# Kernel tuning notes

Hardware: AMD Instinct MI355X
Metric: run time of the kernel (lower is better)

## Reference

```python
import jax, jax.numpy as jnp
import numpy as np

B, D_IN, D_H = 4096, 1024, 2048


def setup_inputs() -> dict:
    key = jax.random.key(0)
    ks = jax.random.split(key, 16)
    s_in = 1.0 / np.sqrt(D_IN)
    s_h = 1.0 / np.sqrt(D_H)
    inp = {
        "x": jax.random.normal(ks[0], (B, D_IN), jnp.float32),
        "h_prev": jax.random.normal(ks[1], (B, D_H), jnp.float32),
        "c_prev": jax.random.normal(ks[2], (B, D_H), jnp.float32),
        "n_prev": jax.random.uniform(ks[3], (B, D_H), jnp.float32) + 0.5,
        # input-gate weights [D_H, D_IN] (torch Linear layout) + biases
        "Wz": jax.random.uniform(ks[4], (D_H, D_IN), jnp.float32, -s_in, s_in),
        "Wi": jax.random.uniform(ks[5], (D_H, D_IN), jnp.float32, -s_in, s_in),
        "Wf": jax.random.uniform(ks[6], (D_H, D_IN), jnp.float32, -s_in, s_in),
        "Wo": jax.random.uniform(ks[7], (D_H, D_IN), jnp.float32, -s_in, s_in),
        "bz": jax.random.uniform(ks[8], (D_H,), jnp.float32, -s_in, s_in),
        "bi": jax.random.uniform(ks[9], (D_H,), jnp.float32, -s_in, s_in),
        "bf": jax.random.uniform(ks[10], (D_H,), jnp.float32, -s_in, s_in),
        "bo": jax.random.uniform(ks[11], (D_H,), jnp.float32, -s_in, s_in),
        # recurrent weights [D_H, D_H], bias-free
        "Rz": jax.random.uniform(ks[12], (D_H, D_H), jnp.float32, -s_h, s_h),
        "Ri": jax.random.uniform(ks[13], (D_H, D_H), jnp.float32, -s_h, s_h),
        "Rf": jax.random.uniform(ks[14], (D_H, D_H), jnp.float32, -s_h, s_h),
        "Ro": jax.random.uniform(ks[15], (D_H, D_H), jnp.float32, -s_h, s_h),
    }
    return inp


def reference(x, h_prev, c_prev, n_prev,
              Wz, Wi, Wf, Wo, bz, bi, bf, bo,
              Rz, Ri, Rf, Ro):
    # Fuse the 4 input GEMMs and 4 recurrent GEMMs into two batched contractions.
    Wcat = jnp.concatenate([Wz, Wi, Wf, Wo], axis=0)      # [4H, D_IN]
    Rcat = jnp.concatenate([Rz, Ri, Rf, Ro], axis=0)      # [4H, H]
    bcat = jnp.concatenate([bz, bi, bf, bo], axis=0)      # [4H]
    pre = x @ Wcat.T + h_prev @ Rcat.T + bcat              # [B, 4H]
    az, ai, af, ao = jnp.split(pre, 4, axis=1)
    z = jnp.tanh(az)
    i = jnp.exp(ai)
    f = jnp.exp(af)
    o = jax.nn.sigmoid(ao)
    c = f * c_prev + i * z
    n = f * n_prev + i
    h = o * (c / n)
    return h
```

## Files before the change

### kernel.cpp

```cpp
#include <hip/hip_runtime.h>
#include <hip/hip_fp16.h>

#define B_SZ  4096
#define DIN   1024
#define DH    2048
#define K_TOT 3072
#define N_TOT 8192

#define BM 128
#define BN 128
#define BK 32

typedef _Float16 half8 __attribute__((ext_vector_type(8)));
typedef float   float4v __attribute__((ext_vector_type(4)));

__device__ __forceinline__ void load_lds16(const void* g, void* l) {
    __builtin_amdgcn_global_load_lds(
        (const __attribute__((address_space(1))) void*)g,
        (__attribute__((address_space(3))) void*)l,
        16, 0, 0);
}

__global__ __launch_bounds__(256) void cast_A_kernel(
        const float* __restrict__ x, const float* __restrict__ h,
        _Float16* __restrict__ A) {
    int idx = (blockIdx.x * 256 + threadIdx.x) * 8;
    int b = idx / K_TOT;
    int c = idx - b * K_TOT;
    const float* src = (c < DIN) ? (x + (size_t)b * DIN + c)
                                 : (h + (size_t)b * DH + (c - DIN));
    float4 v0 = *reinterpret_cast<const float4*>(src);
    float4 v1 = *reinterpret_cast<const float4*>(src + 4);
    half8 o;
    o[0] = (_Float16)v0.x; o[1] = (_Float16)v0.y;
    o[2] = (_Float16)v0.z; o[3] = (_Float16)v0.w;
    o[4] = (_Float16)v1.x; o[5] = (_Float16)v1.y;
    o[6] = (_Float16)v1.z; o[7] = (_Float16)v1.w;
    *reinterpret_cast<half8*>(A + idx) = o;
}

__global__ __launch_bounds__(256) void cast_W_kernel(
        const float* __restrict__ Wz, const float* __restrict__ Wi,
        const float* __restrict__ Wf, const float* __restrict__ Wo,
        const float* __restrict__ Rz, const float* __restrict__ Ri,
        const float* __restrict__ Rf, const float* __restrict__ Ro,
        _Float16* __restrict__ Wb) {
    int idx = (blockIdx.x * 256 + threadIdx.x) * 8;
    int n = idx / K_TOT;
    int c = idx - n * K_TOT;
    int t = n & 127;
    int g = (t >> 4) & 3;
    int j = ((n >> 7) << 5) + ((t >> 6) << 4) + (t & 15);
    const float* W = (g == 0) ? Wz : (g == 1) ? Wi : (g == 2) ? Wf : Wo;
    const float* R = (g == 0) ? Rz : (g == 1) ? Ri : (g == 2) ? Rf : Ro;
    const float* src = (c < DIN) ? (W + (size_t)j * DIN + c)
                                 : (R + (size_t)j * DH + (c - DIN));
    float4 v0 = *reinterpret_cast<const float4*>(src);
    float4 v1 = *reinterpret_cast<const float4*>(src + 4);
    half8 o;
    o[0] = (_Float16)v0.x; o[1] = (_Float16)v0.y;
    o[2] = (_Float16)v0.z; o[3] = (_Float16)v0.w;
    o[4] = (_Float16)v1.x; o[5] = (_Float16)v1.y;
    o[6] = (_Float16)v1.z; o[7] = (_Float16)v1.w;
    *reinterpret_cast<half8*>(Wb + idx) = o;
}

__global__ __launch_bounds__(256) void slstm_gemm_kernel(
        const _Float16* __restrict__ A, const _Float16* __restrict__ Wb,
        const float* __restrict__ c_prev, const float* __restrict__ n_prev,
        const float* __restrict__ bz, const float* __restrict__ bi,
        const float* __restrict__ bf, const float* __restrict__ bo,
        float* __restrict__ Hout) {
    __shared__ __align__(16) _Float16 As[BM * BK];
    __shared__ __align__(16) _Float16 Bs[BN * BK];

    const int ntile = blockIdx.x;
    const int mtile = blockIdx.y;
    const int tid  = threadIdx.x;
    const int wv   = tid >> 6;
    const int wm   = wv >> 1;
    const int wn   = wv & 1;
    const int l    = tid & 63;
    const int quad = l >> 4;
    const int l16  = l & 15;

    const int m0 = mtile * BM;
    const int n0 = ntile * BN;

    float4v acc[4][4];
#pragma unroll
    for (int i = 0; i < 4; i++)
#pragma unroll
        for (int j = 0; j < 4; j++) acc[i][j] = (float4v){0.f, 0.f, 0.f, 0.f};

    const int chunk0 = wv * 2;
    const int srow0  = chunk0 * 16 + (l >> 2);
    const int srow1  = srow0 + 16;
    const int skoff  = (((l & 3) ^ ((l >> 3) & 3)) * 8);

    const _Float16* Ag0 = A  + (size_t)(m0 + srow0) * K_TOT + skoff;
    const _Float16* Ag1 = A  + (size_t)(m0 + srow1) * K_TOT + skoff;
    const _Float16* Bg0 = Wb + (size_t)(n0 + srow0) * K_TOT + skoff;
    const _Float16* Bg1 = Wb + (size_t)(n0 + srow1) * K_TOT + skoff;

    _Float16* AsL0 = As + chunk0 * 512;
    _Float16* AsL1 = As + (chunk0 + 1) * 512;
    _Float16* BsL0 = Bs + chunk0 * 512;
    _Float16* BsL1 = Bs + (chunk0 + 1) * 512;

    const int kq = (quad ^ ((l16 >> 1) & 3)) * 8;

    for (int kt = 0; kt < K_TOT; kt += BK) {
        load_lds16(Ag0 + kt, AsL0);
        load_lds16(Ag1 + kt, AsL1);
        load_lds16(Bg0 + kt, BsL0);
        load_lds16(Bg1 + kt, BsL1);
        __syncthreads();

        half8 afr[4], bfr[4];
#pragma unroll
        for (int mf = 0; mf < 4; mf++)
            afr[mf] = *reinterpret_cast<const half8*>(As + (wm * 64 + mf * 16 + l16) * BK + kq);
#pragma unroll
        for (int nf = 0; nf < 4; nf++)
            bfr[nf] = *reinterpret_cast<const half8*>(Bs + (wn * 64 + nf * 16 + l16) * BK + kq);

#pragma unroll
        for (int mf = 0; mf < 4; mf++)
#pragma unroll
            for (int nf = 0; nf < 4; nf++)
                acc[mf][nf] = __builtin_amdgcn_mfma_f32_16x16x32_f16(afr[mf], bfr[nf], acc[mf][nf], 0, 0, 0);
        __syncthreads();
    }

    const int j = ntile * 32 + wn * 16 + l16;
    const float bzv = bz[j], biv = bi[j], bfv = bf[j], bov = bo[j];
#pragma unroll
    for (int mf = 0; mf < 4; mf++) {
#pragma unroll
        for (int r = 0; r < 4; r++) {
            const int row = m0 + wm * 64 + mf * 16 + quad * 4 + r;
            const size_t off = (size_t)row * DH + j;
            const float az  = acc[mf][0][r] + bzv;
            const float ai  = acc[mf][1][r] + biv;
            const float af_ = acc[mf][2][r] + bfv;
            const float ao  = acc[mf][3][r] + bov;
            const float ax = fabsf(az);
            const float e2 = __expf(-2.0f * ax);
            float tz = __fdividef(1.0f - e2, 1.0f + e2);
            tz = (az >= 0.0f) ? tz : -tz;
            const float iv = __expf(ai);
            const float fv = __expf(af_);
            const float ov = __fdividef(1.0f, 1.0f + __expf(-ao));
            const float cc = fv * c_prev[off] + iv * tz;
            const float nn = fv * n_prev[off] + iv;
            Hout[off] = ov * __fdividef(cc, nn);
        }
    }
}

extern "C" void kernel_launch(void* const* d_in, const int* in_sizes, int n_in,
                              void* d_out, int out_size, void* d_ws, size_t ws_size,
                              hipStream_t stream) {
    const float* x      = (const float*)d_in[0];
    const float* h_prev = (const float*)d_in[1];
    const float* c_prev = (const float*)d_in[2];
    const float* n_prev = (const float*)d_in[3];
    const float* Wz = (const float*)d_in[4];
    const float* Wi = (const float*)d_in[5];
    const float* Wf = (const float*)d_in[6];
    const float* Wo = (const float*)d_in[7];
    const float* bz = (const float*)d_in[8];
    const float* bi = (const float*)d_in[9];
    const float* bf = (const float*)d_in[10];
    const float* bo = (const float*)d_in[11];
    const float* Rz = (const float*)d_in[12];
    const float* Ri = (const float*)d_in[13];
    const float* Rf = (const float*)d_in[14];
    const float* Ro = (const float*)d_in[15];

    _Float16* A  = (_Float16*)d_ws;
    _Float16* Wb = A + (size_t)B_SZ * K_TOT;

    cast_A_kernel<<<(B_SZ * K_TOT / 8) / 256, 256, 0, stream>>>(x, h_prev, A);
    cast_W_kernel<<<(N_TOT * K_TOT / 8) / 256, 256, 0, stream>>>(
        Wz, Wi, Wf, Wo, Rz, Ri, Rf, Ro, Wb);

    dim3 grid(N_TOT / BN, B_SZ / BM);
    slstm_gemm_kernel<<<grid, 256, 0, stream>>>(
        A, Wb, c_prev, n_prev, bz, bi, bf, bo, (float*)d_out);
}
```

Measured before the change: 478.6 us.

## Double GEMM K-tile to 64 with 8-way swizzle and merge cast kernels

The GEMM K-step grows from 32 to 64. Each wave now issues four direct-to-LDS loads per operand, and a new 8-way XOR swizzle matches the wider rows. This halves the number of barrier pairs per K sweep and gives each sync twice as many MFMAs, at the cost of doubling LDS use (32KB per block). The two fp32-to-fp16 cast kernels are also merged into one launch, removing a kernel boundary.

```diff
diff --git a/kernel.cpp b/kernel.cpp
--- a/kernel.cpp
+++ b/kernel.cpp
@@ -9,7 +9,7 @@
 
 #define BM 128
 #define BN 128
-#define BK 32
+#define BK 64
 
 typedef _Float16 half8 __attribute__((ext_vector_type(8)));
 typedef float   float4v __attribute__((ext_vector_type(4)));
@@ -21,14 +21,36 @@
         16, 0, 0);
 }
 
-__global__ __launch_bounds__(256) void cast_A_kernel(
+#define A_BLOCKS ((B_SZ * K_TOT / 8) / 256)
+#define W_BLOCKS ((N_TOT * K_TOT / 8) / 256)
+
+__global__ __launch_bounds__(256) void cast_all_kernel(
         const float* __restrict__ x, const float* __restrict__ h,
-        _Float16* __restrict__ A) {
-    int idx = (blockIdx.x * 256 + threadIdx.x) * 8;
-    int b = idx / K_TOT;
-    int c = idx - b * K_TOT;
-    const float* src = (c < DIN) ? (x + (size_t)b * DIN + c)
-                                 : (h + (size_t)b * DH + (c - DIN));
+        const float* __restrict__ Wz, const float* __restrict__ Wi,
+        const float* __restrict__ Wf, const float* __restrict__ Wo,
+        const float* __restrict__ Rz, const float* __restrict__ Ri,
+        const float* __restrict__ Rf, const float* __restrict__ Ro,
+        _Float16* __restrict__ A, _Float16* __restrict__ Wb) {
+    const float* src;
+    _Float16* dst;
+    if (blockIdx.x < A_BLOCKS) {
+        int idx = (blockIdx.x * 256 + threadIdx.x) * 8;
+        int b = idx / K_TOT;
+        int c = idx - b * K_TOT;
+        src = (c < DIN) ? (x + (size_t)b * DIN + c) : (h + (size_t)b * DH + (c - DIN));
+        dst = A + idx;
+    } else {
+        int idx = ((blockIdx.x - A_BLOCKS) * 256 + threadIdx.x) * 8;
+        int n = idx / K_TOT;
+        int c = idx - n * K_TOT;
+        int t = n & 127;
+        int g = (t >> 4) & 3;
+        int j = ((n >> 7) << 5) + ((t >> 6) << 4) + (t & 15);
+        const float* W = (g == 0) ? Wz : (g == 1) ? Wi : (g == 2) ? Wf : Wo;
+        const float* R = (g == 0) ? Rz : (g == 1) ? Ri : (g == 2) ? Rf : Ro;
+        src = (c < DIN) ? (W + (size_t)j * DIN + c) : (R + (size_t)j * DH + (c - DIN));
+        dst = Wb + idx;
+    }
     float4 v0 = *reinterpret_cast<const float4*>(src);
     float4 v1 = *reinterpret_cast<const float4*>(src + 4);
     half8 o;
@@ -36,33 +58,7 @@
     o[2] = (_Float16)v0.z; o[3] = (_Float16)v0.w;
     o[4] = (_Float16)v1.x; o[5] = (_Float16)v1.y;
     o[6] = (_Float16)v1.z; o[7] = (_Float16)v1.w;
-    *reinterpret_cast<half8*>(A + idx) = o;
-}
-
-__global__ __launch_bounds__(256) void cast_W_kernel(
-        const float* __restrict__ Wz, const float* __restrict__ Wi,
-        const float* __restrict__ Wf, const float* __restrict__ Wo,
-        const float* __restrict__ Rz, const float* __restrict__ Ri,
-        const float* __restrict__ Rf, const float* __restrict__ Ro,
-        _Float16* __restrict__ Wb) {
-    int idx = (blockIdx.x * 256 + threadIdx.x) * 8;
-    int n = idx / K_TOT;
-    int c = idx - n * K_TOT;
-    int t = n & 127;
-    int g = (t >> 4) & 3;
-    int j = ((n >> 7) << 5) + ((t >> 6) << 4) + (t & 15);
-    const float* W = (g == 0) ? Wz : (g == 1) ? Wi : (g == 2) ? Wf : Wo;
-    const float* R = (g == 0) ? Rz : (g == 1) ? Ri : (g == 2) ? Rf : Ro;
-    const float* src = (c < DIN) ? (W + (size_t)j * DIN + c)
-                                 : (R + (size_t)j * DH + (c - DIN));
-    float4 v0 = *reinterpret_cast<const float4*>(src);
-    float4 v1 = *reinterpret_cast<const float4*>(src + 4);
-    half8 o;
-    o[0] = (_Float16)v0.x; o[1] = (_Float16)v0.y;
-    o[2] = (_Float16)v0.z; o[3] = (_Float16)v0.w;
-    o[4] = (_Float16)v1.x; o[5] = (_Float16)v1.y;
-    o[6] = (_Float16)v1.z; o[7] = (_Float16)v1.w;
-    *reinterpret_cast<half8*>(Wb + idx) = o;
+    *reinterpret_cast<half8*>(dst) = o;
 }
 
 __global__ __launch_bounds__(256) void slstm_gemm_kernel(
@@ -93,43 +89,59 @@
 #pragma unroll
         for (int j = 0; j < 4; j++) acc[i][j] = (float4v){0.f, 0.f, 0.f, 0.f};
 
-    const int chunk0 = wv * 2;
-    const int srow0  = chunk0 * 16 + (l >> 2);
-    const int srow1  = srow0 + 16;
-    const int skoff  = (((l & 3) ^ ((l >> 3) & 3)) * 8);
-
-    const _Float16* Ag0 = A  + (size_t)(m0 + srow0) * K_TOT + skoff;
-    const _Float16* Ag1 = A  + (size_t)(m0 + srow1) * K_TOT + skoff;
-    const _Float16* Bg0 = Wb + (size_t)(n0 + srow0) * K_TOT + skoff;
-    const _Float16* Bg1 = Wb + (size_t)(n0 + srow1) * K_TOT + skoff;
-
-    _Float16* AsL0 = As + chunk0 * 512;
-    _Float16* AsL1 = As + (chunk0 + 1) * 512;
-    _Float16* BsL0 = Bs + chunk0 * 512;
-    _Float16* BsL1 = Bs + (chunk0 + 1) * 512;
-
-    const int kq = (quad ^ ((l16 >> 1) & 3)) * 8;
+    const int lrow  = l >> 3;
+    const int skoff = (((l & 7) ^ (lrow & 7)) * 8);
+
+    const int r0 = wv * 32 + lrow;
+    const _Float16* Ag0 = A  + (size_t)(m0 + r0)      * K_TOT + skoff;
+    const _Float16* Ag1 = A  + (size_t)(m0 + r0 + 8)  * K_TOT + skoff;
+    const _Float16* Ag2 = A  + (size_t)(m0 + r0 + 16) * K_TOT + skoff;
+    const _Float16* Ag3 = A  + (size_t)(m0 + r0 + 24) * K_TOT + skoff;
+    const _Float16* Bg0 = Wb + (size_t)(n0 + r0)      * K_TOT + skoff;
+    const _Float16* Bg1 = Wb + (size_t)(n0 + r0 + 8)  * K_TOT + skoff;
+    const _Float16* Bg2 = Wb + (size_t)(n0 + r0 + 16) * K_TOT + skoff;
+    const _Float16* Bg3 = Wb + (size_t)(n0 + r0 + 24) * K_TOT + skoff;
+
+    _Float16* AsL0 = As + (wv * 4 + 0) * 512;
+    _Float16* AsL1 = As + (wv * 4 + 1) * 512;
+    _Float16* AsL2 = As + (wv * 4 + 2) * 512;
+    _Float16* AsL3 = As + (wv * 4 + 3) * 512;
+    _Float16* BsL0 = Bs + (wv * 4 + 0) * 512;
+    _Float16* BsL1 = Bs + (wv * 4 + 1) * 512;
+    _Float16* BsL2 = Bs + (wv * 4 + 2) * 512;
+    _Float16* BsL3 = Bs + (wv * 4 + 3) * 512;
+
+    const int kq0 = (((0 * 4 + quad) ^ (l16 & 7)) * 8);
+    const int kq1 = (((1 * 4 + quad) ^ (l16 & 7)) * 8);
 
     for (int kt = 0; kt < K_TOT; kt += BK) {
         load_lds16(Ag0 + kt, AsL0);
         load_lds16(Ag1 + kt, AsL1);
+        load_lds16(Ag2 + kt, AsL2);
+        load_lds16(Ag3 + kt, AsL3);
         load_lds16(Bg0 + kt, BsL0);
         load_lds16(Bg1 + kt, BsL1);
+        load_lds16(Bg2 + kt, BsL2);
+        load_lds16(Bg3 + kt, BsL3);
         __syncthreads();
 
-        half8 afr[4], bfr[4];
-#pragma unroll
-        for (int mf = 0; mf < 4; mf++)
-            afr[mf] = *reinterpret_cast<const half8*>(As + (wm * 64 + mf * 16 + l16) * BK + kq);
-#pragma unroll
-        for (int nf = 0; nf < 4; nf++)
-            bfr[nf] = *reinterpret_cast<const half8*>(Bs + (wn * 64 + nf * 16 + l16) * BK + kq);
-
-#pragma unroll
-        for (int mf = 0; mf < 4; mf++)
+#pragma unroll
+        for (int kp = 0; kp < 2; kp++) {
+            const int kq = kp ? kq1 : kq0;
+            half8 afr[4], bfr[4];
+#pragma unroll
+            for (int mf = 0; mf < 4; mf++)
+                afr[mf] = *reinterpret_cast<const half8*>(As + (wm * 64 + mf * 16 + l16) * BK + kq);
 #pragma unroll
             for (int nf = 0; nf < 4; nf++)
-                acc[mf][nf] = __builtin_amdgcn_mfma_f32_16x16x32_f16(afr[mf], bfr[nf], acc[mf][nf], 0, 0, 0);
+                bfr[nf] = *reinterpret_cast<const half8*>(Bs + (wn * 64 + nf * 16 + l16) * BK + kq);
+
+#pragma unroll
+            for (int mf = 0; mf < 4; mf++)
+#pragma unroll
+                for (int nf = 0; nf < 4; nf++)
+                    acc[mf][nf] = __builtin_amdgcn_mfma_f32_16x16x32_f16(afr[mf], bfr[nf], acc[mf][nf], 0, 0, 0);
+        }
         __syncthreads();
     }
 
@@ -182,9 +194,8 @@
     _Float16* A  = (_Float16*)d_ws;
     _Float16* Wb = A + (size_t)B_SZ * K_TOT;
 
-    cast_A_kernel<<<(B_SZ * K_TOT / 8) / 256, 256, 0, stream>>>(x, h_prev, A);
-    cast_W_kernel<<<(N_TOT * K_TOT / 8) / 256, 256, 0, stream>>>(
-        Wz, Wi, Wf, Wo, Rz, Ri, Rf, Ro, Wb);
+    cast_all_kernel<<<A_BLOCKS + W_BLOCKS, 256, 0, stream>>>(
+        x, h_prev, Wz, Wi, Wf, Wo, Rz, Ri, Rf, Ro, A, Wb);
 
     dim3 grid(N_TOT / BN, B_SZ / BM);
     slstm_gemm_kernel<<<grid, 256, 0, stream>>>(
```

New measurement: 452.4 us. 1.06x faster.
